# Kernel optimization log

Hardware: AMD Instinct MI355X
Metric: run time of the kernel (lower is better)

Reference implementation:

```python
import jax, jax.numpy as jnp
import numpy as np

B, D, L, H = 8192, 1024, 64, 256

def setup_inputs() -> dict:
    key = jax.random.key(0)
    k_x, k_w1, k_b1, k_w2, k_b2 = jax.random.split(key, 5)
    # Stacked per-label parameters (equivalent to L independent 2-layer MLPs)
    lim1 = 1.0 / np.sqrt(D)
    lim2 = 1.0 / np.sqrt(H)
    return {
        "x": jax.random.normal(k_x, (B, D), dtype=jnp.float32),
        "W1": jax.random.uniform(k_w1, (L, D, H), dtype=jnp.float32, minval=-lim1, maxval=lim1),
        "b1": jax.random.uniform(k_b1, (L, H), dtype=jnp.float32, minval=-lim1, maxval=lim1),
        "W2": jax.random.uniform(k_w2, (L, H), dtype=jnp.float32, minval=-lim2, maxval=lim2),
        "b2": jax.random.uniform(k_b2, (L,), dtype=jnp.float32, minval=-lim2, maxval=lim2),
    }

def reference(x, W1, b1, W2, b2):
    # h: [B, L, H] = relu(x @ W1_l + b1_l) for every label l, as one batched GEMM
    h = jax.nn.relu(jnp.einsum('bd,ldh->blh', x, W1) + b1[None, :, :])
    # out: [B, L] = h_l @ W2_l + b2_l  (second Linear has output dim 1, squeezed)
    out = jnp.einsum('blh,lh->bl', h, W2) + b2[None, :]
    return out
```

## Files before the change

### kernel.cpp

```cpp
#include <hip/hip_runtime.h>
#include <stdint.h>

#define B_SZ 8192
#define D_SZ 1024
#define L_SZ 64
#define H_SZ 256

#define BM 256
#define BN 256
#define BK 64

typedef __attribute__((ext_vector_type(8))) __bf16 bf16x8;
typedef __attribute__((ext_vector_type(4))) float f32x4;

typedef __attribute__((address_space(1))) void as1_void;
typedef __attribute__((address_space(3))) void as3_void;

static __device__ __forceinline__ void gload_lds16(const void* g, void* l) {
    __builtin_amdgcn_global_load_lds((as1_void*)g, (as3_void*)l, 16, 0, 0);
}

static __device__ __forceinline__ unsigned short f2bf(float f) {
    uint32_t u = __builtin_bit_cast(uint32_t, f);
    u += 0x7fffu + ((u >> 16) & 1u);
    return (unsigned short)(u >> 16);
}

__global__ void cvt_x_kernel(const float* __restrict__ x, unsigned short* __restrict__ xb) {
    int i = blockIdx.x * blockDim.x + threadIdx.x;
    const float4 v = reinterpret_cast<const float4*>(x)[i];
    ushort4 o;
    o.x = f2bf(v.x); o.y = f2bf(v.y); o.z = f2bf(v.z); o.w = f2bf(v.w);
    reinterpret_cast<ushort4*>(xb)[i] = o;
}

__global__ void transpose_w1_kernel(const float* __restrict__ w1, unsigned short* __restrict__ w1t) {
    __shared__ float tile[64][65];
    int b = blockIdx.x;
    int l  = b >> 6;
    int dt = (b >> 2) & 15;
    int ht = b & 3;
    int tx = threadIdx.x & 63;
    int ty = threadIdx.x >> 6;
    const float* src = w1 + (size_t)l * (D_SZ * H_SZ);
    #pragma unroll
    for (int r = 0; r < 64; r += 4)
        tile[r + ty][tx] = src[(size_t)(dt * 64 + r + ty) * H_SZ + ht * 64 + tx];
    __syncthreads();
    unsigned short* dst = w1t + (size_t)l * (H_SZ * D_SZ);
    #pragma unroll
    for (int r = 0; r < 64; r += 4)
        dst[(size_t)(ht * 64 + r + ty) * D_SZ + dt * 64 + tx] = f2bf(tile[tx][r + ty]);
}


#define SBAR asm volatile("s_barrier" ::: "memory")
#define VMW(n) asm volatile("s_waitcnt vmcnt(" #n ")" ::: "memory")

#define DS_READ_A(c, quad) do { \
    _Pragma("unroll") for (int j = 0; j < 2; ++j) { \
        const int rowh = ((quad)*2 + j)*16 + rl; \
        _Pragma("unroll") for (int ks = 0; ks < 2; ++ks) { \
            const int slot = (ks*4 + g) ^ (rowh & 7); \
            af[ks][j] = *reinterpret_cast<const bf16x8*>( \
                reinterpret_cast<const char*>(&ldsAB[c][0][wr][0]) + rowh*128 + slot*16); \
        } } } while(0)

#define DS_READ_B(c) do { \
    _Pragma("unroll") for (int nf = 0; nf < 4; ++nf) { \
        const int rowb = wc*64 + nf*16 + rl; \
        const int bh = rowb >> 7; \
        const int rowh = rowb & 127; \
        _Pragma("unroll") for (int ks = 0; ks < 2; ++ks) { \
            const int slot = (ks*4 + g) ^ (rowh & 7); \
            bf[ks][nf] = *reinterpret_cast<const bf16x8*>( \
                reinterpret_cast<const char*>(&ldsAB[c][1][bh][0]) + rowh*128 + slot*16); \
        } } } while(0)

#define MFMA_QUAD(quad) do { \
    __builtin_amdgcn_s_setprio(1); \
    _Pragma("unroll") for (int ks = 0; ks < 2; ++ks) \
    _Pragma("unroll") for (int j = 0; j < 2; ++j) \
    _Pragma("unroll") for (int nf = 0; nf < 4; ++nf) \
        acc[(quad)*2 + j][nf] = __builtin_amdgcn_mfma_f32_16x16x32_bf16( \
            af[ks][j], bf[ks][nf], acc[(quad)*2 + j][nf], 0, 0, 0); \
    __builtin_amdgcn_s_setprio(0); } while(0)

#define STAGE_A(t, h) do { \
    gload_lds16(aSrc[h][0] + (size_t)(t)*BK, &ldsAB[(t)&1][0][h][(wid*64)*8]); \
    gload_lds16(aSrc[h][1] + (size_t)(t)*BK, &ldsAB[(t)&1][0][h][(512 + wid*64)*8]); } while(0)

#define STAGE_AN(h) do { \
    gload_lds16(aSrc[h][0] + ADV, &ldsAB[0][0][h][(wid*64)*8]); \
    gload_lds16(aSrc[h][1] + ADV, &ldsAB[0][0][h][(512 + wid*64)*8]); } while(0)

#define STAGE_B(t, h) do { \
    gload_lds16(bSrc[h][0] + (size_t)(t)*BK, &ldsAB[(t)&1][1][h][(wid*64)*8]); \
    gload_lds16(bSrc[h][1] + (size_t)(t)*BK, &ldsAB[(t)&1][1][h][(512 + wid*64)*8]); } while(0)

__global__ __launch_bounds__(512, 2) void ffn_gemm_kernel(
    const unsigned short* __restrict__ xb,
    const unsigned short* __restrict__ w1t,
    const float* __restrict__ b1,
    const float* __restrict__ w2,
    const float* __restrict__ b2,
    float* __restrict__ out)
{
    __shared__ unsigned short ldsAB[2][2][2][128 * 64];
    __shared__ float partLds[256][4];

    const int bid = blockIdx.x;
    const int l   = (bid & 7) * 8 + ((bid >> 3) & 7);
    const int gi  = bid >> 6;
    const int m00 = gi * 8 * BM;

    const int tid  = threadIdx.x;
    const int wid  = tid >> 6;
    const int lane = tid & 63;
    const int wr   = wid >> 2;
    const int wc   = wid & 3;
    const int g    = lane >> 4;
    const int rl   = lane & 15;

    const size_t ADV = (size_t)BM * D_SZ;

    const unsigned short* aSrc[2][2];
    const unsigned short* bSrc[2][2];
    #pragma unroll
    for (int h = 0; h < 2; ++h)
        #pragma unroll
        for (int c2 = 0; c2 < 2; ++c2) {
            const int q  = c2 * 512 + tid;
            const int r  = q >> 3;
            const int kg = (q & 7) ^ (r & 7);
            aSrc[h][c2] = xb  + (size_t)(m00 + h * 128 + r) * D_SZ + kg * 8;
            bSrc[h][c2] = w1t + ((size_t)l * H_SZ + h * 128 + r) * D_SZ + kg * 8;
        }

    float b1v[4], w2v[4];
    #pragma unroll
    for (int nf = 0; nf < 4; ++nf) {
        const int col = wc * 64 + nf * 16 + rl;
        b1v[nf] = b1[l * H_SZ + col];
        w2v[nf] = w2[l * H_SZ + col];
    }
    const float b2v = b2[l];

    f32x4 acc[8][4];
    bf16x8 af[2][2], bf[2][4];

    STAGE_B(0, 0); STAGE_B(0, 1);
    STAGE_A(0, 0); STAGE_A(0, 1);
    STAGE_B(1, 0); STAGE_B(1, 1);
    VMW(4);
    SBAR;

    #pragma unroll 1
    for (int o = 0; o < 8; ++o) {
        #pragma unroll
        for (int m = 0; m < 8; ++m)
            #pragma unroll
            for (int n = 0; n < 4; ++n) {
                acc[m][n][0] = 0.f; acc[m][n][1] = 0.f;
                acc[m][n][2] = 0.f; acc[m][n][3] = 0.f;
            }

        #pragma unroll 1
        for (int i = 0; i < 7; ++i) {
            const int t1 = 2 * i + 1, t2 = 2 * i + 2, t3 = 2 * i + 3;
            DS_READ_B(0); DS_READ_A(0, 0); STAGE_A(t1, 0); SBAR; MFMA_QUAD(0); SBAR;
            DS_READ_A(0, 1); STAGE_A(t1, 1); SBAR; MFMA_QUAD(1); SBAR;
            DS_READ_A(0, 2); STAGE_B(t2, 0); SBAR; MFMA_QUAD(2); SBAR;
            DS_READ_A(0, 3); STAGE_B(t2, 1); SBAR; MFMA_QUAD(3); VMW(4); SBAR;
            DS_READ_B(1); DS_READ_A(1, 0); STAGE_A(t2, 0); SBAR; MFMA_QUAD(0); SBAR;
            DS_READ_A(1, 1); STAGE_A(t2, 1); SBAR; MFMA_QUAD(1); SBAR;
            DS_READ_A(1, 2); STAGE_B(t3, 0); SBAR; MFMA_QUAD(2); SBAR;
            DS_READ_A(1, 3); STAGE_B(t3, 1); SBAR; MFMA_QUAD(3); VMW(4); SBAR;
        }
        DS_READ_B(0); DS_READ_A(0, 0); STAGE_A(15, 0); SBAR; MFMA_QUAD(0); SBAR;
        DS_READ_A(0, 1); STAGE_A(15, 1); SBAR; MFMA_QUAD(1); SBAR;
        DS_READ_A(0, 2); STAGE_B(0, 0); SBAR; MFMA_QUAD(2); SBAR;
        DS_READ_A(0, 3); STAGE_B(0, 1); SBAR; MFMA_QUAD(3); VMW(4); SBAR;
        DS_READ_B(1); DS_READ_A(1, 0); STAGE_AN(0); SBAR; MFMA_QUAD(0); SBAR;
        DS_READ_A(1, 1); STAGE_AN(1); SBAR; MFMA_QUAD(1); SBAR;
        DS_READ_A(1, 2); STAGE_B(1, 0); SBAR; MFMA_QUAD(2); SBAR;
        DS_READ_A(1, 3); STAGE_B(1, 1); SBAR; MFMA_QUAD(3); VMW(4); SBAR;

        const int m0 = m00 + o * BM;
        #pragma unroll
        for (int mf = 0; mf < 8; ++mf) {
            #pragma unroll
            for (int r = 0; r < 4; ++r) {
                float p = 0.f;
                #pragma unroll
                for (int nf = 0; nf < 4; ++nf) {
                    float v = acc[mf][nf][r] + b1v[nf];
                    v = fmaxf(v, 0.f);
                    p += v * w2v[nf];
                }
                p += __shfl_xor(p, 1);
                p += __shfl_xor(p, 2);
                p += __shfl_xor(p, 4);
                p += __shfl_xor(p, 8);
                if (rl == 0)
                    partLds[wr * 128 + mf * 16 + g * 4 + r][wc] = p;
            }
        }
        __syncthreads();
        if (tid < BM) {
            float s = b2v;
            #pragma unroll
            for (int w = 0; w < 4; ++w) s += partLds[tid][w];
            out[(size_t)(m0 + tid) * L_SZ + l] = s;
        }
        __syncthreads();

        #pragma unroll
        for (int h = 0; h < 2; ++h)
            #pragma unroll
            for (int c2 = 0; c2 < 2; ++c2)
                aSrc[h][c2] += ADV;
    }
    VMW(0);
}

extern "C" void kernel_launch(void* const* d_in, const int* in_sizes, int n_in,
                              void* d_out, int out_size, void* d_ws, size_t ws_size,
                              hipStream_t stream) {
    const float* x  = (const float*)d_in[0];
    const float* W1 = (const float*)d_in[1];
    const float* b1 = (const float*)d_in[2];
    const float* W2 = (const float*)d_in[3];
    const float* b2 = (const float*)d_in[4];
    float* out = (float*)d_out;

    unsigned short* xb  = (unsigned short*)d_ws;
    unsigned short* w1t = xb + (size_t)B_SZ * D_SZ;

    cvt_x_kernel<<<(B_SZ * D_SZ / 4) / 256, 256, 0, stream>>>(x, xb);
    transpose_w1_kernel<<<L_SZ * 16 * 4, 256, 0, stream>>>(W1, w1t);
    ffn_gemm_kernel<<<256, 512, 0, stream>>>(xb, w1t, b1, W2, b2, out);
}
```

Before: 305.6 us.

## Write GEMM output transposed and double-buffer epilogue partials to drop a barrier

The GEMM epilogue now writes each label's results contiguously into a transposed [L,B] workspace instead of strided stores into [B,L]. A new small kernel transposes the result back to the required layout. The per-tile partial-sum buffer is double-buffered by tile parity, which replaces the two __syncthreads with one lgkmcnt wait plus a barrier. This trades an extra kernel launch and a 2 MB round trip for coalesced stores and fewer synchronisations.

Result: no change. 307.7 us (+0.7%).

```diff
diff --git a/kernel.cpp b/kernel.cpp
--- a/kernel.cpp
+++ b/kernel.cpp
@@ -53,9 +53,23 @@
         dst[(size_t)(ht * 64 + r + ty) * D_SZ + dt * 64 + tx] = f2bf(tile[tx][r + ty]);
 }
 
+__global__ void transpose_out_kernel(const float* __restrict__ outT, float* __restrict__ out) {
+    __shared__ float tile[64][65];
+    int b0 = blockIdx.x * 64;
+    int tx = threadIdx.x & 63, ty = threadIdx.x >> 6;
+    #pragma unroll
+    for (int r = 0; r < 64; r += 4)
+        tile[r + ty][tx] = outT[(size_t)(r + ty) * B_SZ + b0 + tx];
+    __syncthreads();
+    #pragma unroll
+    for (int r = 0; r < 64; r += 4)
+        out[(size_t)(b0 + r + ty) * L_SZ + tx] = tile[tx][r + ty];
+}
+
 
 #define SBAR asm volatile("s_barrier" ::: "memory")
 #define VMW(n) asm volatile("s_waitcnt vmcnt(" #n ")" ::: "memory")
+#define LGKM0 asm volatile("s_waitcnt lgkmcnt(0)" ::: "memory")
 
 #define DS_READ_A(c, quad) do { \
     _Pragma("unroll") for (int j = 0; j < 2; ++j) { \
@@ -104,10 +118,10 @@
     const float* __restrict__ b1,
     const float* __restrict__ w2,
     const float* __restrict__ b2,
-    float* __restrict__ out)
+    float* __restrict__ outT)
 {
     __shared__ unsigned short ldsAB[2][2][2][128 * 64];
-    __shared__ float partLds[256][4];
+    __shared__ float partLds[2][4][256];
 
     const int bid = blockIdx.x;
     const int l   = (bid & 7) * 8 + ((bid >> 3) & 7);
@@ -186,34 +200,36 @@
         DS_READ_A(1, 2); STAGE_B(1, 0); SBAR; MFMA_QUAD(2); SBAR;
         DS_READ_A(1, 3); STAGE_B(1, 1); SBAR; MFMA_QUAD(3); VMW(4); SBAR;
 
-        const int m0 = m00 + o * BM;
-        #pragma unroll
-        for (int mf = 0; mf < 8; ++mf) {
+        {
+            const int pp = o & 1;
             #pragma unroll
-            for (int r = 0; r < 4; ++r) {
-                float p = 0.f;
+            for (int mf = 0; mf < 8; ++mf) {
                 #pragma unroll
-                for (int nf = 0; nf < 4; ++nf) {
-                    float v = acc[mf][nf][r] + b1v[nf];
-                    v = fmaxf(v, 0.f);
-                    p += v * w2v[nf];
+                for (int r = 0; r < 4; ++r) {
+                    float p = 0.f;
+                    #pragma unroll
+                    for (int nf = 0; nf < 4; ++nf) {
+                        float v = acc[mf][nf][r] + b1v[nf];
+                        v = fmaxf(v, 0.f);
+                        p += v * w2v[nf];
+                    }
+                    p += __shfl_xor(p, 1);
+                    p += __shfl_xor(p, 2);
+                    p += __shfl_xor(p, 4);
+                    p += __shfl_xor(p, 8);
+                    if (rl == 0)
+                        partLds[pp][wc][wr * 128 + mf * 16 + g * 4 + r] = p;
                 }
-                p += __shfl_xor(p, 1);
-                p += __shfl_xor(p, 2);
-                p += __shfl_xor(p, 4);
-                p += __shfl_xor(p, 8);
-                if (rl == 0)
-                    partLds[wr * 128 + mf * 16 + g * 4 + r][wc] = p;
+            }
+            LGKM0;
+            SBAR;
+            if (tid < BM) {
+                float s = b2v;
+                #pragma unroll
+                for (int w = 0; w < 4; ++w) s += partLds[pp][w][tid];
+                outT[(size_t)l * B_SZ + m00 + o * BM + tid] = s;
             }
         }
-        __syncthreads();
-        if (tid < BM) {
-            float s = b2v;
-            #pragma unroll
-            for (int w = 0; w < 4; ++w) s += partLds[tid][w];
-            out[(size_t)(m0 + tid) * L_SZ + l] = s;
-        }
-        __syncthreads();
 
         #pragma unroll
         for (int h = 0; h < 2; ++h)
@@ -236,8 +252,10 @@
 
     unsigned short* xb  = (unsigned short*)d_ws;
     unsigned short* w1t = xb + (size_t)B_SZ * D_SZ;
+    float* outT = (float*)(w1t + (size_t)L_SZ * H_SZ * D_SZ);
 
     cvt_x_kernel<<<(B_SZ * D_SZ / 4) / 256, 256, 0, stream>>>(x, xb);
     transpose_w1_kernel<<<L_SZ * 16 * 4, 256, 0, stream>>>(W1, w1t);
-    ffn_gemm_kernel<<<256, 512, 0, stream>>>(xb, w1t, b1, W2, b2, out);
-}
+    ffn_gemm_kernel<<<256, 512, 0, stream>>>(xb, w1t, b1, W2, b2, outT);
+    transpose_out_kernel<<<B_SZ / 64, 256, 0, stream>>>(outT, out);
+}
```
